# Optimization experiments

Hardware: AMD Instinct MI355X
Metric: run time of the kernel (lower is better)

Reference implementation:

```python
import jax, jax.numpy as jnp
import numpy as np

NEG_FILL = -1.0e9
PROB_MIN = 1e-9


def _lstm_cell(x, h, c, w_ih, w_hh, b_ih, b_hh):
    # PyTorch gate order: input, forget, cell(g), output
    gates = x @ w_ih.T + h @ w_hh.T + b_ih + b_hh
    i, f, g, o = jnp.split(gates, 4, axis=-1)
    c_new = jax.nn.sigmoid(f) * c + jax.nn.sigmoid(i) * jnp.tanh(g)
    h_new = jax.nn.sigmoid(o) * jnp.tanh(c_new)
    return h_new, c_new


def setup_inputs() -> dict:
    key = jax.random.key(0)
    B, T, D, H, W = 2048, 100, 128, 256, 256
    ks = jax.random.split(key, 16)
    s_d = 1.0 / np.sqrt(D)
    s_h = 1.0 / np.sqrt(H)
    s_w = 1.0 / np.sqrt(W)
    return {
        "targets": jax.random.normal(ks[0], (B, T, D), jnp.float32),
        "h0": jax.random.normal(ks[1], (1, B, H), jnp.float32),
        "c0": jax.random.normal(ks[2], (1, B, H), jnp.float32),
        "enc_w_ih": jax.random.normal(ks[3], (4 * H, D), jnp.float32) * s_d,
        "enc_w_hh": jax.random.normal(ks[4], (4 * H, H), jnp.float32) * s_h,
        "enc_b_ih": jax.random.normal(ks[5], (4 * H,), jnp.float32) * s_h,
        "enc_b_hh": jax.random.normal(ks[6], (4 * H,), jnp.float32) * s_h,
        "dec_w_ih": jax.random.normal(ks[7], (4 * H, D), jnp.float32) * s_d,
        "dec_w_hh": jax.random.normal(ks[8], (4 * H, H), jnp.float32) * s_h,
        "dec_b_ih": jax.random.normal(ks[9], (4 * H,), jnp.float32) * s_h,
        "dec_b_hh": jax.random.normal(ks[10], (4 * H,), jnp.float32) * s_h,
        "W1": jax.random.normal(ks[11], (W, H), jnp.float32) * s_h,
        "W2": jax.random.normal(ks[12], (W, H), jnp.float32) * s_h,
        "vt": jax.random.normal(ks[13], (W,), jnp.float32) * s_w,
    }


def reference(targets, h0, c0, enc_w_ih, enc_w_hh, enc_b_ih, enc_b_hh,
              dec_w_ih, dec_w_hh, dec_b_ih, dec_b_hh, W1, W2, vt):
    B, T, D = targets.shape
    H = enc_w_hh.shape[1]

    # ---- encoder LSTM (batch_first, zero initial state) ----
    def enc_step(carry, x_t):
        h, c = carry
        h, c = _lstm_cell(x_t, h, c, enc_w_ih, enc_w_hh, enc_b_ih, enc_b_hh)
        return (h, c), h

    z = jnp.zeros((B, H), targets.dtype)
    _, enc_h = jax.lax.scan(enc_step, (z, z), jnp.swapaxes(targets, 0, 1))
    encoder_states = jnp.swapaxes(enc_h, 0, 1)  # [B, T, H]

    blend1 = encoder_states @ W1.T  # [B, T, W]

    a1 = jnp.arange(B)
    init = (h0[0], c0[0], jnp.zeros((B, T), dtype=bool), jnp.zeros_like(targets[:, 0]))

    def dec_step(carry, _):
        h, c, selected, dec_in = carry
        h, c = _lstm_cell(dec_in, h, c, dec_w_ih, dec_w_hh, dec_b_ih, dec_b_hh)
        blend2 = h @ W2.T                                   # [B, W]
        scores = jnp.tanh(blend1 + blend2[:, None, :]) @ vt  # [B, T]
        scores = jnp.where(selected, NEG_FILL, scores)
        sel = jnp.argmax(scores, axis=-1)                    # [B]
        selected = selected.at[a1, sel].set(True)
        probs = jnp.maximum(jax.nn.softmax(scores, axis=-1), PROB_MIN)
        dec_in = targets[a1, sel]                            # [B, D]
        return (h, c, selected, dec_in), probs

    _, probs = jax.lax.scan(dec_step, init, None, length=T)
    return jnp.swapaxes(probs, 0, 1)  # [B, T, T]
```

## Files before the change

### kernel.cpp

```cpp
#include <hip/hip_runtime.h>
#include <math.h>
#include <stdint.h>

#define BB   2048
#define TT   100
#define DD   128
#define HH   256
#define NEGF -1.0e9f

typedef __attribute__((ext_vector_type(8))) short short8_t;
typedef __attribute__((ext_vector_type(4))) float f32x4;

#define MFMA16(a,b,c) __builtin_amdgcn_mfma_f32_16x16x32_bf16((a),(b),(c),0,0,0)

__device__ __forceinline__ float sigmoidf_(float x){ return 1.0f/(1.0f+expf(-x)); }

__device__ __forceinline__ float tanh_fast(float x){
  x = fminf(15.f, fmaxf(-15.f, x));
  const float e = __expf(x + x);
  return (e - 1.f) * __builtin_amdgcn_rcpf(e + 1.f);
}

__device__ __forceinline__ void bf16_split3(float x, unsigned short &h,
                                            unsigned short &m, unsigned short &l){
  const unsigned u = __float_as_uint(x);
  const unsigned r = u + 0x7FFFu + ((u >> 16) & 1u);
  h = (unsigned short)(r >> 16);
  const float rem = x - __uint_as_float(r & 0xFFFF0000u);
  const unsigned u2 = __float_as_uint(rem);
  const unsigned r2 = u2 + 0x7FFFu + ((u2 >> 16) & 1u);
  m = (unsigned short)(r2 >> 16);
  const float rem2 = rem - __uint_as_float(r2 & 0xFFFF0000u);
  l = (unsigned short)(__float_as_uint(rem2) >> 16);
}

__global__ __launch_bounds__(256) void k_split3(const float* __restrict__ src,
    unsigned short* __restrict__ hi, unsigned short* __restrict__ mi,
    unsigned short* __restrict__ lo, int n){
  const int i = blockIdx.x*256 + threadIdx.x;
  if(i < n){ unsigned short h,m,l; bf16_split3(src[i], h, m, l);
             hi[i]=h; mi[i]=m; lo[i]=l; }
}

__global__ __launch_bounds__(256) void k_zero_i32(int* __restrict__ p, int n){
  int i = blockIdx.x*256 + threadIdx.x;
  if(i < n) p[i] = 0;
}

#define MFMA_X6(aH,aM,aL,bH,bM,bL,acc)            \
  do{ acc = MFMA16(aM, bM, acc);                  \
      acc = MFMA16(aH, bL, acc);                  \
      acc = MFMA16(aL, bH, acc);                  \
      acc = MFMA16(aH, bM, acc);                  \
      acc = MFMA16(aM, bH, acc);                  \
      acc = MFMA16(aH, bH, acc); }while(0)

__global__ __launch_bounds__(128) void k_gates_cell(
    const float* __restrict__ Xp, int ldx,
    const float* __restrict__ Hp,
    const unsigned short* __restrict__ WihH, const unsigned short* __restrict__ WihM,
    const unsigned short* __restrict__ WihL,
    const unsigned short* __restrict__ WhhH, const unsigned short* __restrict__ WhhM,
    const unsigned short* __restrict__ WhhL,
    const float* __restrict__ bih, const float* __restrict__ bhh,
    const float* __restrict__ Cp,
    float* __restrict__ Hout, float* __restrict__ Cout,
    float* __restrict__ Hcopy, int hstride)
{
  __shared__ alignas(16) unsigned short AsH[64*40], AsM[64*40], AsL[64*40];
  __shared__ alignas(16) unsigned short WsH[64*40], WsM[64*40], WsL[64*40];
  const int tid  = threadIdx.x;
  const int lane = tid & 63;
  const int wv   = tid >> 6;
  const int l15  = lane & 15;
  const int l4   = lane >> 4;
  const int j0   = blockIdx.x * 16;
  const int m0   = blockIdx.y * 64;

  f32x4 acc[2][4];
  #pragma unroll
  for(int a=0;a<2;a++)
    #pragma unroll
    for(int s=0;s<4;s++)
      #pragma unroll
      for(int e=0;e<4;e++) acc[a][s][e] = 0.f;

  for(int phase=0; phase<2; phase++){
    const float* Am; int lda;
    const unsigned short *WH, *WM, *WL; int ldw, nt;
    if(phase==0){ if(!Xp) continue; Am=Xp; lda=ldx;
                  WH=WihH; WM=WihM; WL=WihL; ldw=DD; nt=4; }
    else        { if(!Hp) continue; Am=Hp; lda=HH;
                  WH=WhhH; WM=WhhM; WL=WhhL; ldw=HH; nt=8; }
    for(int kt=0; kt<nt; kt++){
      const int k0 = kt*32;
      __syncthreads();
      #pragma unroll
      for(int it=0; it<4; it++){
        const int q  = it*128 + tid;
        const int r  = q >> 3;
        const int kq = (q & 7) << 2;
        const float4 v = *(const float4*)(Am + (size_t)(m0+r)*lda + k0 + kq);
        unsigned short h0,m0_,l0,h1,m1_,l1,h2,m2_,l2,h3,m3_,l3;
        bf16_split3(v.x,h0,m0_,l0); bf16_split3(v.y,h1,m1_,l1);
        bf16_split3(v.z,h2,m2_,l2); bf16_split3(v.w,h3,m3_,l3);
        *(ushort4*)&AsH[r*40+kq] = make_ushort4(h0,h1,h2,h3);
        *(ushort4*)&AsM[r*40+kq] = make_ushort4(m0_,m1_,m2_,m3_);
        *(ushort4*)&AsL[r*40+kq] = make_ushort4(l0,l1,l2,l3);
      }
      #pragma unroll
      for(int half=0; half<3; half++){
        const unsigned short* __restrict__ Wg = (half==0)?WH:((half==1)?WM:WL);
        unsigned short* Ws = (half==0)?WsH:((half==1)?WsM:WsL);
        #pragma unroll
        for(int it=0; it<2; it++){
          const int q  = it*128 + tid;
          const int c  = q >> 2;
          const int kq = (q & 3) << 3;
          const int n  = ((c>>4)*HH) + j0 + (c & 15);
          *(uint4*)&Ws[c*40+kq] = *(const uint4*)(Wg + (size_t)n*ldw + k0 + kq);
        }
      }
      __syncthreads();
      short8_t aH[2], aM[2], aL[2];
      #pragma unroll
      for(int fm=0; fm<2; fm++){
        const int r = wv*32 + fm*16 + l15;
        aH[fm] = *(const short8_t*)&AsH[r*40 + l4*8];
        aM[fm] = *(const short8_t*)&AsM[r*40 + l4*8];
        aL[fm] = *(const short8_t*)&AsL[r*40 + l4*8];
      }
      #pragma unroll
      for(int s=0; s<4; s++){
        const int c = s*16 + l15;
        const short8_t bH = *(const short8_t*)&WsH[c*40 + l4*8];
        const short8_t bM = *(const short8_t*)&WsM[c*40 + l4*8];
        const short8_t bL = *(const short8_t*)&WsL[c*40 + l4*8];
        #pragma unroll
        for(int fm=0; fm<2; fm++){
          MFMA_X6(aH[fm],aM[fm],aL[fm], bH,bM,bL, acc[fm][s]);
        }
      }
    }
  }

  const int j = j0 + l15;
  const float bi0 = bih[       j] + bhh[       j];
  const float bf0 = bih[  HH + j] + bhh[  HH + j];
  const float bg0 = bih[2*HH + j] + bhh[2*HH + j];
  const float bo0 = bih[3*HH + j] + bhh[3*HH + j];
  #pragma unroll
  for(int fm=0; fm<2; fm++){
    #pragma unroll
    for(int r=0; r<4; r++){
      const int m = m0 + wv*32 + fm*16 + l4*4 + r;
      const size_t idx = (size_t)m*HH + j;
      const float iv = acc[fm][0][r] + bi0;
      const float fv = acc[fm][1][r] + bf0;
      const float gv = acc[fm][2][r] + bg0;
      const float ov = acc[fm][3][r] + bo0;
      const float cp = Cp ? Cp[idx] : 0.f;
      const float cn = sigmoidf_(fv)*cp + sigmoidf_(iv)*tanhf(gv);
      const float hn = sigmoidf_(ov)*tanhf(cn);
      Cout[idx] = cn;
      Hout[idx] = hn;
      if(Hcopy) Hcopy[(size_t)m*hstride + j] = hn;
    }
  }
}

__global__ __launch_bounds__(128) void k_blend2(
    const float* __restrict__ Hin,
    const unsigned short* __restrict__ W2H, const unsigned short* __restrict__ W2M,
    const unsigned short* __restrict__ W2L,
    float* __restrict__ out)
{
  __shared__ alignas(16) unsigned short AsH[32*40], AsM[32*40], AsL[32*40];
  __shared__ alignas(16) unsigned short WsH[64*40], WsM[64*40], WsL[64*40];
  const int tid  = threadIdx.x;
  const int lane = tid & 63;
  const int wv   = tid >> 6;
  const int l15  = lane & 15;
  const int l4   = lane >> 4;
  const int n0   = blockIdx.x * 64;
  const int m0   = blockIdx.y * 32;

  f32x4 acc[4];
  #pragma unroll
  for(int s=0;s<4;s++)
    #pragma unroll
    for(int e=0;e<4;e++) acc[s][e] = 0.f;

  for(int kt=0; kt<8; kt++){
    const int k0 = kt*32;
    __syncthreads();
    #pragma unroll
    for(int it=0; it<2; it++){
      const int q  = it*128 + tid;
      const int r  = q >> 3;
      const int kq = (q & 7) << 2;
      const float4 v = *(const float4*)(Hin + (size_t)(m0+r)*HH + k0 + kq);
      unsigned short h0,m0_,l0,h1,m1_,l1,h2,m2_,l2,h3,m3_,l3;
      bf16_split3(v.x,h0,m0_,l0); bf16_split3(v.y,h1,m1_,l1);
      bf16_split3(v.z,h2,m2_,l2); bf16_split3(v.w,h3,m3_,l3);
      *(ushort4*)&AsH[r*40+kq] = make_ushort4(h0,h1,h2,h3);
      *(ushort4*)&AsM[r*40+kq] = make_ushort4(m0_,m1_,m2_,m3_);
      *(ushort4*)&AsL[r*40+kq] = make_ushort4(l0,l1,l2,l3);
    }
    #pragma unroll
    for(int half=0; half<3; half++){
      const unsigned short* __restrict__ Wg = (half==0)?W2H:((half==1)?W2M:W2L);
      unsigned short* Ws = (half==0)?WsH:((half==1)?WsM:WsL);
      #pragma unroll
      for(int it=0; it<2; it++){
        const int q  = it*128 + tid;
        const int c  = q >> 2;
        const int kq = (q & 3) << 3;
        const int n  = n0 + c;
        *(uint4*)&Ws[c*40+kq] = *(const uint4*)(Wg + (size_t)n*HH + k0 + kq);
      }
    }
    __syncthreads();
    const int r = wv*16 + l15;
    const short8_t aH = *(const short8_t*)&AsH[r*40 + l4*8];
    const short8_t aM = *(const short8_t*)&AsM[r*40 + l4*8];
    const short8_t aL = *(const short8_t*)&AsL[r*40 + l4*8];
    #pragma unroll
    for(int s=0; s<4; s++){
      const int c = s*16 + l15;
      const short8_t bH = *(const short8_t*)&WsH[c*40 + l4*8];
      const short8_t bM = *(const short8_t*)&WsM[c*40 + l4*8];
      const short8_t bL = *(const short8_t*)&WsL[c*40 + l4*8];
      MFMA_X6(aH,aM,aL, bH,bM,bL, acc[s]);
    }
  }
  #pragma unroll
  for(int s=0; s<4; s++)
    #pragma unroll
    for(int r=0; r<4; r++)
      out[(size_t)(m0 + wv*16 + l4*4 + r)*HH + n0 + s*16 + l15] = acc[s][r];
}

__global__ __launch_bounds__(128) void k_blend1(
    float* __restrict__ blend1,
    const unsigned short* __restrict__ W1H, const unsigned short* __restrict__ W1M,
    const unsigned short* __restrict__ W1L)
{
  __shared__ alignas(16) unsigned short AsH[32*264], AsM[32*264], AsL[32*264];
  const int tid  = threadIdx.x;
  const int lane = tid & 63;
  const int wv   = tid >> 6;
  const int l15  = lane & 15;
  const int l4   = lane >> 4;
  const size_t r0 = (size_t)blockIdx.x * 32;

  #pragma unroll
  for(int it=0; it<16; it++){
    const int q  = it*128 + tid;
    const int r  = q >> 6;
    const int kq = (q & 63) << 2;
    const float4 v = *(const float4*)(blend1 + (r0+r)*256 + kq);
    unsigned short h0,m0_,l0,h1,m1_,l1,h2,m2_,l2,h3,m3_,l3;
    bf16_split3(v.x,h0,m0_,l0); bf16_split3(v.y,h1,m1_,l1);
    bf16_split3(v.z,h2,m2_,l2); bf16_split3(v.w,h3,m3_,l3);
    *(ushort4*)&AsH[r*264+kq] = make_ushort4(h0,h1,h2,h3);
    *(ushort4*)&AsM[r*264+kq] = make_ushort4(m0_,m1_,m2_,m3_);
    *(ushort4*)&AsL[r*264+kq] = make_ushort4(l0,l1,l2,l3);
  }
  __syncthreads();

  f32x4 acc[16];
  #pragma unroll
  for(int s=0;s<16;s++)
    #pragma unroll
    for(int e=0;e<4;e++) acc[s][e] = 0.f;

  const int rb = wv*16;
  for(int kt=0; kt<8; kt++){
    const int k0 = kt*32;
    const short8_t aH = *(const short8_t*)&AsH[(rb+l15)*264 + k0 + l4*8];
    const short8_t aM = *(const short8_t*)&AsM[(rb+l15)*264 + k0 + l4*8];
    const short8_t aL = *(const short8_t*)&AsL[(rb+l15)*264 + k0 + l4*8];
    #pragma unroll
    for(int fn=0; fn<16; fn++){
      const int n = fn*16 + l15;
      const short8_t bH = *(const short8_t*)(W1H + (size_t)n*256 + k0 + l4*8);
      const short8_t bM = *(const short8_t*)(W1M + (size_t)n*256 + k0 + l4*8);
      const short8_t bL = *(const short8_t*)(W1L + (size_t)n*256 + k0 + l4*8);
      MFMA_X6(aH,aM,aL, bH,bM,bL, acc[fn]);
    }
  }
  #pragma unroll
  for(int fn=0; fn<16; fn++)
    #pragma unroll
    for(int r=0; r<4; r++)
      blend1[(r0 + rb + l4*4 + r)*256 + fn*16 + l15] = acc[fn][r];
}

__global__ __launch_bounds__(256) void k_scores(
    const float* __restrict__ blend1,
    const float* __restrict__ blend2,
    const float* __restrict__ vt,
    const float* __restrict__ targets,
    int*  __restrict__ selected,
    float* __restrict__ dec_in,
    float* __restrict__ out,
    int s)
{
  __shared__ float vt_s[256], b2_s[256], sc[128];
  __shared__ float M_s, S_s;
  __shared__ int sel_s;
  const int b = blockIdx.x;
  const int tid = threadIdx.x;
  const int lane = tid & 63;
  const int wave = tid >> 6;

  vt_s[tid] = vt[tid];
  b2_s[tid] = blend2[(size_t)b*256 + tid];
  __syncthreads();

  const float4 bb = *(const float4*)&b2_s[lane*4];
  const float4 vv = *(const float4*)&vt_s[lane*4];

  for(int it=0; it<25; it++){
    const int t = wave + it*4;
    const float4 x = *(const float4*)(blend1 + ((size_t)b*TT + t)*256 + lane*4);
    float p;
    p = tanh_fast(x.x + bb.x) * vv.x;
    p = fmaf(tanh_fast(x.y + bb.y), vv.y, p);
    p = fmaf(tanh_fast(x.z + bb.z), vv.z, p);
    p = fmaf(tanh_fast(x.w + bb.w), vv.w, p);
    #pragma unroll
    for(int off=32; off>=1; off>>=1) p += __shfl_xor(p, off, 64);
    if(lane == 0) sc[t] = p;
  }
  __syncthreads();

  if(wave == 0){
    float m1 = selected[(size_t)b*TT + lane] ? NEGF : sc[lane];
    sc[lane] = m1;
    float bestv = m1; int besti = lane;
    float m2 = 0.f;
    const int t2 = lane + 64;
    if(t2 < TT){
      m2 = selected[(size_t)b*TT + t2] ? NEGF : sc[t2];
      sc[t2] = m2;
      if(m2 > bestv){ bestv = m2; besti = t2; }
    }
    #pragma unroll
    for(int off=32; off>=1; off>>=1){
      const float ov = __shfl_xor(bestv, off, 64);
      const int   oi = __shfl_xor(besti, off, 64);
      if(ov > bestv || (ov == bestv && oi < besti)){ bestv = ov; besti = oi; }
    }
    float e = __expf(m1 - bestv);
    if(t2 < TT) e += __expf(m2 - bestv);
    #pragma unroll
    for(int off=32; off>=1; off>>=1) e += __shfl_xor(e, off, 64);
    if(lane == 0){
      M_s = bestv; S_s = e; sel_s = besti;
      selected[(size_t)b*TT + besti] = 1;
    }
  }
  __syncthreads();

  const int sel = sel_s;
  if(tid < TT){
    float p = __expf(sc[tid] - M_s) / S_s;
    out[(size_t)b*TT*TT + (size_t)s*TT + tid] = fmaxf(p, 1e-9f);
  }
  if(tid < DD){
    dec_in[(size_t)b*DD + tid] = targets[((size_t)b*TT + sel)*DD + tid];
  }
}

extern "C" void kernel_launch(void* const* d_in, const int* in_sizes, int n_in,
                              void* d_out, int out_size, void* d_ws, size_t ws_size,
                              hipStream_t stream)
{
  (void)in_sizes; (void)n_in; (void)out_size; (void)ws_size;
  const float* targets  = (const float*)d_in[0];
  const float* h0       = (const float*)d_in[1];
  const float* c0       = (const float*)d_in[2];
  const float* enc_w_ih = (const float*)d_in[3];
  const float* enc_w_hh = (const float*)d_in[4];
  const float* enc_b_ih = (const float*)d_in[5];
  const float* enc_b_hh = (const float*)d_in[6];
  const float* dec_w_ih = (const float*)d_in[7];
  const float* dec_w_hh = (const float*)d_in[8];
  const float* dec_b_ih = (const float*)d_in[9];
  const float* dec_b_hh = (const float*)d_in[10];
  const float* W1       = (const float*)d_in[11];
  const float* W2       = (const float*)d_in[12];
  const float* vt       = (const float*)d_in[13];
  float* out = (float*)d_out;

  float* ws      = (float*)d_ws;
  float* blend1  = ws;
  float* hA      = blend1 + (size_t)BB*TT*256;
  float* hB      = hA + (size_t)BB*HH;
  float* cA      = hB + (size_t)BB*HH;
  float* cB      = cA + (size_t)BB*HH;
  float* blend2  = cB + (size_t)BB*HH;
  float* dec_in  = blend2 + (size_t)BB*HH;
  int*   selected= (int*)(dec_in + (size_t)BB*DD);

  char* pc = (char*)(selected + (size_t)BB*TT);
  pc = (char*)(((uintptr_t)pc + 63) & ~(uintptr_t)63);
  unsigned short* q = (unsigned short*)pc;
  unsigned short* ewihH = q; q += (size_t)1024*128;
  unsigned short* ewihM = q; q += (size_t)1024*128;
  unsigned short* ewihL = q; q += (size_t)1024*128;
  unsigned short* ewhhH = q; q += (size_t)1024*256;
  unsigned short* ewhhM = q; q += (size_t)1024*256;
  unsigned short* ewhhL = q; q += (size_t)1024*256;
  unsigned short* dwihH = q; q += (size_t)1024*128;
  unsigned short* dwihM = q; q += (size_t)1024*128;
  unsigned short* dwihL = q; q += (size_t)1024*128;
  unsigned short* dwhhH = q; q += (size_t)1024*256;
  unsigned short* dwhhM = q; q += (size_t)1024*256;
  unsigned short* dwhhL = q; q += (size_t)1024*256;
  unsigned short* w1H   = q; q += (size_t)256*256;
  unsigned short* w1M   = q; q += (size_t)256*256;
  unsigned short* w1L   = q; q += (size_t)256*256;
  unsigned short* w2H   = q; q += (size_t)256*256;
  unsigned short* w2M   = q; q += (size_t)256*256;
  unsigned short* w2L   = q; q += (size_t)256*256;

  k_split3<<<(1024*128+255)/256, 256, 0, stream>>>(enc_w_ih, ewihH, ewihM, ewihL, 1024*128);
  k_split3<<<(1024*256+255)/256, 256, 0, stream>>>(enc_w_hh, ewhhH, ewhhM, ewhhL, 1024*256);
  k_split3<<<(1024*128+255)/256, 256, 0, stream>>>(dec_w_ih, dwihH, dwihM, dwihL, 1024*128);
  k_split3<<<(1024*256+255)/256, 256, 0, stream>>>(dec_w_hh, dwhhH, dwhhM, dwhhL, 1024*256);
  k_split3<<<(256*256+255)/256,  256, 0, stream>>>(W1, w1H, w1M, w1L, 256*256);
  k_split3<<<(256*256+255)/256,  256, 0, stream>>>(W2, w2H, w2M, w2L, 256*256);

  k_zero_i32<<<(BB*TT + 255)/256, 256, 0, stream>>>(selected, BB*TT);

  for(int t=0; t<TT; t++){
    const float* Hp = (t==0) ? nullptr : ((t&1) ? hA : hB);
    const float* Cp = (t==0) ? nullptr : ((t&1) ? cA : cB);
    float* Ho = (t&1) ? hB : hA;
    float* Co = (t&1) ? cB : cA;
    k_gates_cell<<<dim3(16,32), 128, 0, stream>>>(
        targets + (size_t)t*DD, TT*DD,
        Hp, ewihH, ewihM, ewihL, ewhhH, ewhhM, ewhhL, enc_b_ih, enc_b_hh, Cp,
        Ho, Co, blend1 + (size_t)t*256, TT*256);
  }

  k_blend1<<<BB*TT/32, 128, 0, stream>>>(blend1, w1H, w1M, w1L);

  for(int s=0; s<TT; s++){
    const float* Hp = (s==0) ? h0 : ((s&1) ? hA : hB);
    const float* Cp = (s==0) ? c0 : ((s&1) ? cA : cB);
    float* Ho = (s&1) ? hB : hA;
    float* Co = (s&1) ? cB : cA;
    const float* Xp = (s==0) ? nullptr : dec_in;
    k_gates_cell<<<dim3(16,32), 128, 0, stream>>>(
        Xp, DD, Hp, dwihH, dwihM, dwihL, dwhhH, dwhhM, dwhhL, dec_b_ih, dec_b_hh, Cp,
        Ho, Co, nullptr, 0);
    k_blend2<<<dim3(4,64), 128, 0, stream>>>(Ho, w2H, w2M, w2L, blend2);
    k_scores<<<BB, 256, 0, stream>>>(blend1, blend2, vt, targets, selected,
                                     dec_in, out, s);
  }
}
```

Before: 14.68 ms.

## Fuse encoder and decoder time loops into persistent cooperative kernels

```diff
diff --git a/kernel.cpp b/kernel.cpp
--- a/kernel.cpp
+++ b/kernel.cpp
@@ -1,6 +1,9 @@
 #include <hip/hip_runtime.h>
+#include <hip/hip_cooperative_groups.h>
 #include <math.h>
 #include <stdint.h>
+
+namespace cg = cooperative_groups;
 
 #define BB   2048
 #define TT   100
@@ -20,6 +23,8 @@
   const float e = __expf(x + x);
   return (e - 1.f) * __builtin_amdgcn_rcpf(e + 1.f);
 }
+
+__device__ __forceinline__ float b2f(unsigned u){ return __uint_as_float(u << 16); }
 
 __device__ __forceinline__ void bf16_split3(float x, unsigned short &h,
                                             unsigned short &m, unsigned short &l){
@@ -47,6 +52,13 @@
   if(i < n) p[i] = 0;
 }
 
+__global__ __launch_bounds__(256) void k_transpose256(const float* __restrict__ in,
+                                                      float* __restrict__ outp){
+  const int k = blockIdx.x;
+  const int n = threadIdx.x;
+  outp[k*256 + n] = in[n*256 + k];
+}
+
 #define MFMA_X6(aH,aM,aL,bH,bM,bL,acc)            \
   do{ acc = MFMA16(aM, bM, acc);                  \
       acc = MFMA16(aH, bL, acc);                  \
@@ -55,190 +67,376 @@
       acc = MFMA16(aM, bH, acc);                  \
       acc = MFMA16(aH, bH, acc); }while(0)
 
-__global__ __launch_bounds__(128) void k_gates_cell(
-    const float* __restrict__ Xp, int ldx,
-    const float* __restrict__ Hp,
+struct GatesSmem {
+  alignas(16) unsigned short AsH[64*40];
+  alignas(16) unsigned short AsM[64*40];
+  alignas(16) unsigned short AsL[64*40];
+  alignas(16) unsigned short WsH[128*40];
+  alignas(16) unsigned short WsM[128*40];
+  alignas(16) unsigned short WsL[128*40];
+};
+
+__device__ __forceinline__ void stage_W(GatesSmem& sm,
+    const unsigned short* __restrict__ WH, const unsigned short* __restrict__ WM,
+    const unsigned short* __restrict__ WL, int ldw, int j0, int k0, int tid){
+  #pragma unroll
+  for(int half=0; half<3; half++){
+    const unsigned short* __restrict__ Wg = (half==0)?WH:((half==1)?WM:WL);
+    unsigned short* Ws = (half==0)?sm.WsH:((half==1)?sm.WsM:sm.WsL);
+    #pragma unroll
+    for(int it=0; it<2; it++){
+      const int q  = it*256 + tid;
+      const int cc = q >> 2;
+      const int kq = (q & 3) << 3;
+      const int n  = ((cc>>5)*HH) + j0 + (cc & 31);
+      *(uint4*)&Ws[cc*40 + kq] = *(const uint4*)(Wg + (size_t)n*ldw + k0 + kq);
+    }
+  }
+}
+
+__device__ __forceinline__ void stage_A_presplit(GatesSmem& sm,
+    const unsigned short* __restrict__ AH, const unsigned short* __restrict__ AM,
+    const unsigned short* __restrict__ AL, int lda, int m0, int k0, int tid){
+  const int r  = tid >> 2;
+  const int kq = (tid & 3) << 3;
+  const size_t off = (size_t)(m0+r)*lda + k0 + kq;
+  *(uint4*)&sm.AsH[r*40+kq] = *(const uint4*)(AH + off);
+  *(uint4*)&sm.AsM[r*40+kq] = *(const uint4*)(AM + off);
+  *(uint4*)&sm.AsL[r*40+kq] = *(const uint4*)(AL + off);
+}
+
+__device__ __forceinline__ void stage_A_f32(GatesSmem& sm,
+    const float* __restrict__ A, size_t lda, int m0, int k0, int tid){
+  #pragma unroll
+  for(int it=0; it<2; it++){
+    const int q  = it*256 + tid;
+    const int r  = q >> 3;
+    const int kq = (q & 7) << 2;
+    const float4 v = *(const float4*)(A + (size_t)(m0+r)*lda + k0 + kq);
+    unsigned short h0,m0_,l0,h1,m1_,l1,h2,m2_,l2,h3,m3_,l3;
+    bf16_split3(v.x,h0,m0_,l0); bf16_split3(v.y,h1,m1_,l1);
+    bf16_split3(v.z,h2,m2_,l2); bf16_split3(v.w,h3,m3_,l3);
+    *(ushort4*)&sm.AsH[r*40+kq] = make_ushort4(h0,h1,h2,h3);
+    *(ushort4*)&sm.AsM[r*40+kq] = make_ushort4(m0_,m1_,m2_,m3_);
+    *(ushort4*)&sm.AsL[r*40+kq] = make_ushort4(l0,l1,l2,l3);
+  }
+}
+
+__device__ __forceinline__ void gates_compute(GatesSmem& sm, f32x4 (&acc)[2][4],
+                                              int mh, int j16, int l15, int l4){
+  short8_t aH[2], aM[2], aL[2];
+  #pragma unroll
+  for(int fm=0; fm<2; fm++){
+    const int rr = mh*32 + fm*16 + l15;
+    aH[fm] = *(const short8_t*)&sm.AsH[rr*40 + l4*8];
+    aM[fm] = *(const short8_t*)&sm.AsM[rr*40 + l4*8];
+    aL[fm] = *(const short8_t*)&sm.AsL[rr*40 + l4*8];
+  }
+  #pragma unroll
+  for(int s4=0; s4<4; s4++){
+    const int cc = s4*32 + j16 + l15;
+    const short8_t bH = *(const short8_t*)&sm.WsH[cc*40 + l4*8];
+    const short8_t bM = *(const short8_t*)&sm.WsM[cc*40 + l4*8];
+    const short8_t bL = *(const short8_t*)&sm.WsL[cc*40 + l4*8];
+    #pragma unroll
+    for(int fm=0; fm<2; fm++){
+      MFMA_X6(aH[fm],aM[fm],aL[fm], bH,bM,bL, acc[fm][s4]);
+    }
+  }
+}
+
+__global__ __launch_bounds__(256) void k_encoder(
+    const float* __restrict__ targets,
     const unsigned short* __restrict__ WihH, const unsigned short* __restrict__ WihM,
     const unsigned short* __restrict__ WihL,
     const unsigned short* __restrict__ WhhH, const unsigned short* __restrict__ WhhM,
     const unsigned short* __restrict__ WhhL,
     const float* __restrict__ bih, const float* __restrict__ bhh,
-    const float* __restrict__ Cp,
-    float* __restrict__ Hout, float* __restrict__ Cout,
-    float* __restrict__ Hcopy, int hstride)
+    unsigned short* __restrict__ hAH, unsigned short* __restrict__ hAM,
+    unsigned short* __restrict__ hAL,
+    unsigned short* __restrict__ hBH, unsigned short* __restrict__ hBM,
+    unsigned short* __restrict__ hBL,
+    float* __restrict__ cbuf, float* __restrict__ blend1)
 {
-  __shared__ alignas(16) unsigned short AsH[64*40], AsM[64*40], AsL[64*40];
-  __shared__ alignas(16) unsigned short WsH[64*40], WsM[64*40], WsL[64*40];
+  cg::grid_group grid = cg::this_grid();
+  __shared__ GatesSmem sm;
   const int tid  = threadIdx.x;
   const int lane = tid & 63;
   const int wv   = tid >> 6;
   const int l15  = lane & 15;
   const int l4   = lane >> 4;
-  const int j0   = blockIdx.x * 16;
-  const int m0   = blockIdx.y * 64;
-
-  f32x4 acc[2][4];
-  #pragma unroll
-  for(int a=0;a<2;a++)
-    #pragma unroll
-    for(int s=0;s<4;s++)
-      #pragma unroll
-      for(int e=0;e<4;e++) acc[a][s][e] = 0.f;
-
-  for(int phase=0; phase<2; phase++){
-    const float* Am; int lda;
-    const unsigned short *WH, *WM, *WL; int ldw, nt;
-    if(phase==0){ if(!Xp) continue; Am=Xp; lda=ldx;
-                  WH=WihH; WM=WihM; WL=WihL; ldw=DD; nt=4; }
-    else        { if(!Hp) continue; Am=Hp; lda=HH;
-                  WH=WhhH; WM=WhhM; WL=WhhL; ldw=HH; nt=8; }
-    for(int kt=0; kt<nt; kt++){
-      const int k0 = kt*32;
-      __syncthreads();
-      #pragma unroll
-      for(int it=0; it<4; it++){
-        const int q  = it*128 + tid;
-        const int r  = q >> 3;
-        const int kq = (q & 7) << 2;
-        const float4 v = *(const float4*)(Am + (size_t)(m0+r)*lda + k0 + kq);
-        unsigned short h0,m0_,l0,h1,m1_,l1,h2,m2_,l2,h3,m3_,l3;
-        bf16_split3(v.x,h0,m0_,l0); bf16_split3(v.y,h1,m1_,l1);
-        bf16_split3(v.z,h2,m2_,l2); bf16_split3(v.w,h3,m3_,l3);
-        *(ushort4*)&AsH[r*40+kq] = make_ushort4(h0,h1,h2,h3);
-        *(ushort4*)&AsM[r*40+kq] = make_ushort4(m0_,m1_,m2_,m3_);
-        *(ushort4*)&AsL[r*40+kq] = make_ushort4(l0,l1,l2,l3);
-      }
-      #pragma unroll
-      for(int half=0; half<3; half++){
-        const unsigned short* __restrict__ Wg = (half==0)?WH:((half==1)?WM:WL);
-        unsigned short* Ws = (half==0)?WsH:((half==1)?WsM:WsL);
-        #pragma unroll
-        for(int it=0; it<2; it++){
-          const int q  = it*128 + tid;
-          const int c  = q >> 2;
-          const int kq = (q & 3) << 3;
-          const int n  = ((c>>4)*HH) + j0 + (c & 15);
-          *(uint4*)&Ws[c*40+kq] = *(const uint4*)(Wg + (size_t)n*ldw + k0 + kq);
-        }
-      }
-      __syncthreads();
-      short8_t aH[2], aM[2], aL[2];
-      #pragma unroll
-      for(int fm=0; fm<2; fm++){
-        const int r = wv*32 + fm*16 + l15;
-        aH[fm] = *(const short8_t*)&AsH[r*40 + l4*8];
-        aM[fm] = *(const short8_t*)&AsM[r*40 + l4*8];
-        aL[fm] = *(const short8_t*)&AsL[r*40 + l4*8];
-      }
-      #pragma unroll
-      for(int s=0; s<4; s++){
-        const int c = s*16 + l15;
-        const short8_t bH = *(const short8_t*)&WsH[c*40 + l4*8];
-        const short8_t bM = *(const short8_t*)&WsM[c*40 + l4*8];
-        const short8_t bL = *(const short8_t*)&WsL[c*40 + l4*8];
-        #pragma unroll
-        for(int fm=0; fm<2; fm++){
-          MFMA_X6(aH[fm],aM[fm],aL[fm], bH,bM,bL, acc[fm][s]);
-        }
-      }
-    }
-  }
-
-  const int j = j0 + l15;
+  const int bid  = blockIdx.x;
+  const int m0   = (bid >> 3) * 64;
+  const int j0   = (bid & 7) * 32;
+  const int mh   = wv & 1;
+  const int j16  = (wv >> 1) * 16;
+
+  const int j = j0 + j16 + l15;
   const float bi0 = bih[       j] + bhh[       j];
   const float bf0 = bih[  HH + j] + bhh[  HH + j];
   const float bg0 = bih[2*HH + j] + bhh[2*HH + j];
   const float bo0 = bih[3*HH + j] + bhh[3*HH + j];
-  #pragma unroll
-  for(int fm=0; fm<2; fm++){
-    #pragma unroll
-    for(int r=0; r<4; r++){
-      const int m = m0 + wv*32 + fm*16 + l4*4 + r;
-      const size_t idx = (size_t)m*HH + j;
-      const float iv = acc[fm][0][r] + bi0;
-      const float fv = acc[fm][1][r] + bf0;
-      const float gv = acc[fm][2][r] + bg0;
-      const float ov = acc[fm][3][r] + bo0;
-      const float cp = Cp ? Cp[idx] : 0.f;
-      const float cn = sigmoidf_(fv)*cp + sigmoidf_(iv)*tanhf(gv);
-      const float hn = sigmoidf_(ov)*tanhf(cn);
-      Cout[idx] = cn;
-      Hout[idx] = hn;
-      if(Hcopy) Hcopy[(size_t)m*hstride + j] = hn;
-    }
-  }
-}
-
-__global__ __launch_bounds__(128) void k_blend2(
-    const float* __restrict__ Hin,
-    const unsigned short* __restrict__ W2H, const unsigned short* __restrict__ W2M,
-    const unsigned short* __restrict__ W2L,
-    float* __restrict__ out)
+
+  for(int t=0; t<TT; t++){
+    f32x4 acc[2][4];
+    #pragma unroll
+    for(int a=0;a<2;a++)
+      #pragma unroll
+      for(int s=0;s<4;s++)
+        #pragma unroll
+        for(int e=0;e<4;e++) acc[a][s][e] = 0.f;
+
+    for(int kt=0; kt<4; kt++){
+      const int k0 = kt*32;
+      __syncthreads();
+      stage_A_f32(sm, targets + (size_t)t*DD, (size_t)TT*DD, m0, k0, tid);
+      stage_W(sm, WihH, WihM, WihL, DD, j0, k0, tid);
+      __syncthreads();
+      gates_compute(sm, acc, mh, j16, l15, l4);
+    }
+    if(t > 0){
+      const unsigned short* hH = (t&1) ? hAH : hBH;
+      const unsigned short* hM = (t&1) ? hAM : hBM;
+      const unsigned short* hL = (t&1) ? hAL : hBL;
+      for(int kt=0; kt<8; kt++){
+        const int k0 = kt*32;
+        __syncthreads();
+        stage_A_presplit(sm, hH, hM, hL, HH, m0, k0, tid);
+        stage_W(sm, WhhH, WhhM, WhhL, HH, j0, k0, tid);
+        __syncthreads();
+        gates_compute(sm, acc, mh, j16, l15, l4);
+      }
+    }
+    unsigned short* hoH = (t&1) ? hBH : hAH;
+    unsigned short* hoM = (t&1) ? hBM : hAM;
+    unsigned short* hoL = (t&1) ? hBL : hAL;
+    #pragma unroll
+    for(int fm=0; fm<2; fm++){
+      #pragma unroll
+      for(int r=0; r<4; r++){
+        const int m = m0 + mh*32 + fm*16 + l4*4 + r;
+        const size_t idx = (size_t)m*HH + j;
+        const float iv = acc[fm][0][r] + bi0;
+        const float fv = acc[fm][1][r] + bf0;
+        const float gv = acc[fm][2][r] + bg0;
+        const float ov = acc[fm][3][r] + bo0;
+        const float cp = (t==0) ? 0.f : cbuf[idx];
+        const float cn = sigmoidf_(fv)*cp + sigmoidf_(iv)*tanhf(gv);
+        const float hn = sigmoidf_(ov)*tanhf(cn);
+        cbuf[idx] = cn;
+        unsigned short sh, sm_, sl;
+        bf16_split3(hn, sh, sm_, sl);
+        hoH[idx] = sh; hoM[idx] = sm_; hoL[idx] = sl;
+        blend1[(size_t)m*(TT*256) + (size_t)t*256 + j] = hn;
+      }
+    }
+    if(t < TT-1) grid.sync();
+  }
+}
+
+__global__ __launch_bounds__(256) void k_decoder(
+    const float* __restrict__ targets,
+    const unsigned short* __restrict__ WihH, const unsigned short* __restrict__ WihM,
+    const unsigned short* __restrict__ WihL,
+    const unsigned short* __restrict__ WhhH, const unsigned short* __restrict__ WhhM,
+    const unsigned short* __restrict__ WhhL,
+    const float* __restrict__ bih, const float* __restrict__ bhh,
+    const float* __restrict__ c0, float* __restrict__ cbuf,
+    const unsigned short* __restrict__ hAH, const unsigned short* __restrict__ hAM,
+    const unsigned short* __restrict__ hAL,
+    unsigned short* __restrict__ hBH, unsigned short* __restrict__ hBM,
+    unsigned short* __restrict__ hBL,
+    unsigned short* __restrict__ decH, unsigned short* __restrict__ decM,
+    unsigned short* __restrict__ decL,
+    const float* __restrict__ W2t, const float* __restrict__ vt,
+    const float* __restrict__ blend1,
+    int* __restrict__ selected, float* __restrict__ outp)
 {
-  __shared__ alignas(16) unsigned short AsH[32*40], AsM[32*40], AsL[32*40];
-  __shared__ alignas(16) unsigned short WsH[64*40], WsM[64*40], WsL[64*40];
+  cg::grid_group grid = cg::this_grid();
+  __shared__ GatesSmem sm;
+  __shared__ float Hs[8][260];
+  __shared__ float scs[8][104];
   const int tid  = threadIdx.x;
   const int lane = tid & 63;
   const int wv   = tid >> 6;
   const int l15  = lane & 15;
   const int l4   = lane >> 4;
-  const int n0   = blockIdx.x * 64;
-  const int m0   = blockIdx.y * 32;
-
-  f32x4 acc[4];
-  #pragma unroll
-  for(int s=0;s<4;s++)
-    #pragma unroll
-    for(int e=0;e<4;e++) acc[s][e] = 0.f;
-
-  for(int kt=0; kt<8; kt++){
-    const int k0 = kt*32;
+  const int bid  = blockIdx.x;
+  const int m0   = (bid >> 3) * 64;
+  const int j0   = (bid & 7) * 32;
+  const int mh   = wv & 1;
+  const int j16  = (wv >> 1) * 16;
+  const int r0b  = bid * 8;
+
+  const int j = j0 + j16 + l15;
+  const float bi0 = bih[       j] + bhh[       j];
+  const float bf0 = bih[  HH + j] + bhh[  HH + j];
+  const float bg0 = bih[2*HH + j] + bhh[2*HH + j];
+  const float bo0 = bih[3*HH + j] + bhh[3*HH + j];
+  const float4 vv = *(const float4*)(vt + lane*4);
+
+  for(int st=0; st<TT; st++){
+    f32x4 acc[2][4];
+    #pragma unroll
+    for(int a=0;a<2;a++)
+      #pragma unroll
+      for(int s=0;s<4;s++)
+        #pragma unroll
+        for(int e=0;e<4;e++) acc[a][s][e] = 0.f;
+
+    if(st > 0){
+      for(int kt=0; kt<4; kt++){
+        const int k0 = kt*32;
+        __syncthreads();
+        stage_A_presplit(sm, decH, decM, decL, DD, m0, k0, tid);
+        stage_W(sm, WihH, WihM, WihL, DD, j0, k0, tid);
+        __syncthreads();
+        gates_compute(sm, acc, mh, j16, l15, l4);
+      }
+    }
+    {
+      const unsigned short* hH = (st&1) ? hBH : hAH;
+      const unsigned short* hM = (st&1) ? hBM : hAM;
+      const unsigned short* hL = (st&1) ? hBL : hAL;
+      for(int kt=0; kt<8; kt++){
+        const int k0 = kt*32;
+        __syncthreads();
+        stage_A_presplit(sm, hH, hM, hL, HH, m0, k0, tid);
+        stage_W(sm, WhhH, WhhM, WhhL, HH, j0, k0, tid);
+        __syncthreads();
+        gates_compute(sm, acc, mh, j16, l15, l4);
+      }
+    }
+    {
+      unsigned short* hoH = (st&1) ? (unsigned short*)hAH : hBH;
+      unsigned short* hoM = (st&1) ? (unsigned short*)hAM : hBM;
+      unsigned short* hoL = (st&1) ? (unsigned short*)hAL : hBL;
+      const float* csrc = (st==0) ? c0 : cbuf;
+      #pragma unroll
+      for(int fm=0; fm<2; fm++){
+        #pragma unroll
+        for(int r=0; r<4; r++){
+          const int m = m0 + mh*32 + fm*16 + l4*4 + r;
+          const size_t idx = (size_t)m*HH + j;
+          const float iv = acc[fm][0][r] + bi0;
+          const float fv = acc[fm][1][r] + bf0;
+          const float gv = acc[fm][2][r] + bg0;
+          const float ov = acc[fm][3][r] + bo0;
+          const float cp = csrc[idx];
+          const float cn = sigmoidf_(fv)*cp + sigmoidf_(iv)*tanhf(gv);
+          const float hn = sigmoidf_(ov)*tanhf(cn);
+          cbuf[idx] = cn;
+          unsigned short sh, sm_, sl;
+          bf16_split3(hn, sh, sm_, sl);
+          hoH[idx] = sh; hoM[idx] = sm_; hoL[idx] = sl;
+        }
+      }
+    }
+    grid.sync();
+
+    {
+      const unsigned short* hH = (st&1) ? hAH : hBH;
+      const unsigned short* hM = (st&1) ? hAM : hBM;
+      const unsigned short* hL = (st&1) ? hAL : hBL;
+      const int r  = tid >> 5;
+      const int kq = (tid & 31) << 3;
+      const size_t off = (size_t)(r0b + r)*HH + kq;
+      const uint4 uh = *(const uint4*)(hH + off);
+      const uint4 um = *(const uint4*)(hM + off);
+      const uint4 ul = *(const uint4*)(hL + off);
+      #pragma unroll
+      for(int e=0; e<4; e++){
+        const unsigned wh = ((const unsigned*)&uh)[e];
+        const unsigned wm = ((const unsigned*)&um)[e];
+        const unsigned wl = ((const unsigned*)&ul)[e];
+        Hs[r][kq + e*2 + 0] = b2f(wh & 0xffffu) + b2f(wm & 0xffffu) + b2f(wl & 0xffffu);
+        Hs[r][kq + e*2 + 1] = b2f(wh >> 16)     + b2f(wm >> 16)     + b2f(wl >> 16);
+      }
+    }
     __syncthreads();
-    #pragma unroll
-    for(int it=0; it<2; it++){
-      const int q  = it*128 + tid;
-      const int r  = q >> 3;
-      const int kq = (q & 7) << 2;
-      const float4 v = *(const float4*)(Hin + (size_t)(m0+r)*HH + k0 + kq);
-      unsigned short h0,m0_,l0,h1,m1_,l1,h2,m2_,l2,h3,m3_,l3;
-      bf16_split3(v.x,h0,m0_,l0); bf16_split3(v.y,h1,m1_,l1);
-      bf16_split3(v.z,h2,m2_,l2); bf16_split3(v.w,h3,m3_,l3);
-      *(ushort4*)&AsH[r*40+kq] = make_ushort4(h0,h1,h2,h3);
-      *(ushort4*)&AsM[r*40+kq] = make_ushort4(m0_,m1_,m2_,m3_);
-      *(ushort4*)&AsL[r*40+kq] = make_ushort4(l0,l1,l2,l3);
-    }
-    #pragma unroll
-    for(int half=0; half<3; half++){
-      const unsigned short* __restrict__ Wg = (half==0)?W2H:((half==1)?W2M:W2L);
-      unsigned short* Ws = (half==0)?WsH:((half==1)?WsM:WsL);
-      #pragma unroll
-      for(int it=0; it<2; it++){
-        const int q  = it*128 + tid;
-        const int c  = q >> 2;
-        const int kq = (q & 3) << 3;
-        const int n  = n0 + c;
-        *(uint4*)&Ws[c*40+kq] = *(const uint4*)(Wg + (size_t)n*HH + k0 + kq);
-      }
-    }
-    __syncthreads();
-    const int r = wv*16 + l15;
-    const short8_t aH = *(const short8_t*)&AsH[r*40 + l4*8];
-    const short8_t aM = *(const short8_t*)&AsM[r*40 + l4*8];
-    const short8_t aL = *(const short8_t*)&AsL[r*40 + l4*8];
-    #pragma unroll
-    for(int s=0; s<4; s++){
-      const int c = s*16 + l15;
-      const short8_t bH = *(const short8_t*)&WsH[c*40 + l4*8];
-      const short8_t bM = *(const short8_t*)&WsM[c*40 + l4*8];
-      const short8_t bL = *(const short8_t*)&WsL[c*40 + l4*8];
-      MFMA_X6(aH,aM,aL, bH,bM,bL, acc[s]);
-    }
-  }
-  #pragma unroll
-  for(int s=0; s<4; s++)
-    #pragma unroll
-    for(int r=0; r<4; r++)
-      out[(size_t)(m0 + wv*16 + l4*4 + r)*HH + n0 + s*16 + l15] = acc[s][r];
+
+    float bacc[2][4];
+    #pragma unroll
+    for(int r=0;r<2;r++)
+      #pragma unroll
+      for(int cG=0;cG<4;cG++) bacc[r][cG] = 0.f;
+    {
+      const int rA = wv*2, rB = wv*2 + 1;
+      for(int kc=0; kc<64; kc++){
+        const float4 ha = *(const float4*)&Hs[rA][kc*4];
+        const float4 hb = *(const float4*)&Hs[rB][kc*4];
+        const float haa[4] = {ha.x,ha.y,ha.z,ha.w};
+        const float hbb[4] = {hb.x,hb.y,hb.z,hb.w};
+        #pragma unroll
+        for(int i=0;i<4;i++){
+          const float4 w = *(const float4*)(W2t + (size_t)(kc*4+i)*HH + lane*4);
+          bacc[0][0] = fmaf(haa[i], w.x, bacc[0][0]);
+          bacc[0][1] = fmaf(haa[i], w.y, bacc[0][1]);
+          bacc[0][2] = fmaf(haa[i], w.z, bacc[0][2]);
+          bacc[0][3] = fmaf(haa[i], w.w, bacc[0][3]);
+          bacc[1][0] = fmaf(hbb[i], w.x, bacc[1][0]);
+          bacc[1][1] = fmaf(hbb[i], w.y, bacc[1][1]);
+          bacc[1][2] = fmaf(hbb[i], w.z, bacc[1][2]);
+          bacc[1][3] = fmaf(hbb[i], w.w, bacc[1][3]);
+        }
+      }
+    }
+
+    #pragma unroll
+    for(int rr=0; rr<2; rr++){
+      const int r = wv*2 + rr;
+      const int brow = r0b + r;
+      const float4 bb = make_float4(bacc[rr][0], bacc[rr][1], bacc[rr][2], bacc[rr][3]);
+      const float* bl = blend1 + (size_t)brow * (TT*256);
+      #pragma unroll 2
+      for(int t=0; t<TT; t++){
+        const float4 x = *(const float4*)(bl + t*256 + lane*4);
+        float p;
+        p = tanh_fast(x.x + bb.x) * vv.x;
+        p = fmaf(tanh_fast(x.y + bb.y), vv.y, p);
+        p = fmaf(tanh_fast(x.z + bb.z), vv.z, p);
+        p = fmaf(tanh_fast(x.w + bb.w), vv.w, p);
+        #pragma unroll
+        for(int off=32; off>=1; off>>=1) p += __shfl_xor(p, off, 64);
+        if(lane == 0) scs[r][t] = p;
+      }
+      const size_t selbase = (size_t)brow*TT;
+      const float m1 = selected[selbase + lane] ? NEGF : scs[r][lane];
+      float bestv = m1; int besti = lane;
+      const int t2 = lane + 64;
+      float m2 = NEGF;
+      if(t2 < TT){
+        m2 = selected[selbase + t2] ? NEGF : scs[r][t2];
+        if(m2 > bestv){ bestv = m2; besti = t2; }
+      }
+      #pragma unroll
+      for(int off=32; off>=1; off>>=1){
+        const float ov = __shfl_xor(bestv, off, 64);
+        const int   oi = __shfl_xor(besti, off, 64);
+        if(ov > bestv || (ov == bestv && oi < besti)){ bestv = ov; besti = oi; }
+      }
+      float e = __expf(m1 - bestv);
+      if(t2 < TT) e += __expf(m2 - bestv);
+      #pragma unroll
+      for(int off=32; off>=1; off>>=1) e += __shfl_xor(e, off, 64);
+
+      outp[(size_t)brow*(TT*TT) + (size_t)st*TT + lane] = fmaxf(__expf(m1 - bestv)/e, 1e-9f);
+      if(t2 < TT)
+        outp[(size_t)brow*(TT*TT) + (size_t)st*TT + t2] = fmaxf(__expf(m2 - bestv)/e, 1e-9f);
+      if(lane == 0) selected[selbase + besti] = 1;
+      #pragma unroll
+      for(int dd=0; dd<2; dd++){
+        const int d = lane + dd*64;
+        const float xv = targets[((size_t)brow*TT + besti)*DD + d];
+        unsigned short th, tm, tl;
+        bf16_split3(xv, th, tm, tl);
+        decH[(size_t)brow*DD + d] = th;
+        decM[(size_t)brow*DD + d] = tm;
+        decL[(size_t)brow*DD + d] = tl;
+      }
+    }
+    if(st < TT-1) grid.sync();
+  }
 }
 
 __global__ __launch_bounds__(128) void k_blend1(
@@ -295,83 +493,6 @@
     #pragma unroll
     for(int r=0; r<4; r++)
       blend1[(r0 + rb + l4*4 + r)*256 + fn*16 + l15] = acc[fn][r];
-}
-
-__global__ __launch_bounds__(256) void k_scores(
-    const float* __restrict__ blend1,
-    const float* __restrict__ blend2,
-    const float* __restrict__ vt,
-    const float* __restrict__ targets,
-    int*  __restrict__ selected,
-    float* __restrict__ dec_in,
-    float* __restrict__ out,
-    int s)
-{
-  __shared__ float vt_s[256], b2_s[256], sc[128];
-  __shared__ float M_s, S_s;
-  __shared__ int sel_s;
-  const int b = blockIdx.x;
-  const int tid = threadIdx.x;
-  const int lane = tid & 63;
-  const int wave = tid >> 6;
-
-  vt_s[tid] = vt[tid];
-  b2_s[tid] = blend2[(size_t)b*256 + tid];
-  __syncthreads();
-
-  const float4 bb = *(const float4*)&b2_s[lane*4];
-  const float4 vv = *(const float4*)&vt_s[lane*4];
-
-  for(int it=0; it<25; it++){
-    const int t = wave + it*4;
-    const float4 x = *(const float4*)(blend1 + ((size_t)b*TT + t)*256 + lane*4);
-    float p;
-    p = tanh_fast(x.x + bb.x) * vv.x;
-    p = fmaf(tanh_fast(x.y + bb.y), vv.y, p);
-    p = fmaf(tanh_fast(x.z + bb.z), vv.z, p);
-    p = fmaf(tanh_fast(x.w + bb.w), vv.w, p);
-    #pragma unroll
-    for(int off=32; off>=1; off>>=1) p += __shfl_xor(p, off, 64);
-    if(lane == 0) sc[t] = p;
-  }
-  __syncthreads();
-
-  if(wave == 0){
-    float m1 = selected[(size_t)b*TT + lane] ? NEGF : sc[lane];
-    sc[lane] = m1;
-    float bestv = m1; int besti = lane;
-    float m2 = 0.f;
-    const int t2 = lane + 64;
-    if(t2 < TT){
-      m2 = selected[(size_t)b*TT + t2] ? NEGF : sc[t2];
-      sc[t2] = m2;
-      if(m2 > bestv){ bestv = m2; besti = t2; }
-    }
-    #pragma unroll
-    for(int off=32; off>=1; off>>=1){
-      const float ov = __shfl_xor(bestv, off, 64);
-      const int   oi = __shfl_xor(besti, off, 64);
-      if(ov > bestv || (ov == bestv && oi < besti)){ bestv = ov; besti = oi; }
-    }
-    float e = __expf(m1 - bestv);
-    if(t2 < TT) e += __expf(m2 - bestv);
-    #pragma unroll
-    for(int off=32; off>=1; off>>=1) e += __shfl_xor(e, off, 64);
-    if(lane == 0){
-      M_s = bestv; S_s = e; sel_s = besti;
-      selected[(size_t)b*TT + besti] = 1;
-    }
-  }
-  __syncthreads();
-
-  const int sel = sel_s;
-  if(tid < TT){
-    float p = __expf(sc[tid] - M_s) / S_s;
-    out[(size_t)b*TT*TT + (size_t)s*TT + tid] = fmaxf(p, 1e-9f);
-  }
-  if(tid < DD){
-    dec_in[(size_t)b*DD + tid] = targets[((size_t)b*TT + sel)*DD + tid];
-  }
 }
 
 extern "C" void kernel_launch(void* const* d_in, const int* in_sizes, int n_in,
@@ -393,21 +514,22 @@
   const float* W1       = (const float*)d_in[11];
   const float* W2       = (const float*)d_in[12];
   const float* vt       = (const float*)d_in[13];
-  float* out = (float*)d_out;
+  float* outp = (float*)d_out;
 
   float* ws      = (float*)d_ws;
   float* blend1  = ws;
-  float* hA      = blend1 + (size_t)BB*TT*256;
-  float* hB      = hA + (size_t)BB*HH;
-  float* cA      = hB + (size_t)BB*HH;
-  float* cB      = cA + (size_t)BB*HH;
-  float* blend2  = cB + (size_t)BB*HH;
-  float* dec_in  = blend2 + (size_t)BB*HH;
-  int*   selected= (int*)(dec_in + (size_t)BB*DD);
-
+  float* cbuf    = blend1 + (size_t)BB*TT*256;
+  float* W2t     = cbuf + (size_t)BB*HH;
+  int*   selected= (int*)(W2t + 256*256);
   char* pc = (char*)(selected + (size_t)BB*TT);
   pc = (char*)(((uintptr_t)pc + 63) & ~(uintptr_t)63);
   unsigned short* q = (unsigned short*)pc;
+  unsigned short* hsAH = q; q += (size_t)BB*HH;
+  unsigned short* hsAM = q; q += (size_t)BB*HH;
+  unsigned short* hsAL = q; q += (size_t)BB*HH;
+  unsigned short* hsBH = q; q += (size_t)BB*HH;
+  unsigned short* hsBM = q; q += (size_t)BB*HH;
+  unsigned short* hsBL = q; q += (size_t)BB*HH;
   unsigned short* ewihH = q; q += (size_t)1024*128;
   unsigned short* ewihM = q; q += (size_t)1024*128;
   unsigned short* ewihL = q; q += (size_t)1024*128;
@@ -423,43 +545,49 @@
   unsigned short* w1H   = q; q += (size_t)256*256;
   unsigned short* w1M   = q; q += (size_t)256*256;
   unsigned short* w1L   = q; q += (size_t)256*256;
-  unsigned short* w2H   = q; q += (size_t)256*256;
-  unsigned short* w2M   = q; q += (size_t)256*256;
-  unsigned short* w2L   = q; q += (size_t)256*256;
+  unsigned short* decH = ewihH;
+  unsigned short* decM = ewihH + (size_t)BB*DD;
+  unsigned short* decL = ewihH + (size_t)2*BB*DD;
 
   k_split3<<<(1024*128+255)/256, 256, 0, stream>>>(enc_w_ih, ewihH, ewihM, ewihL, 1024*128);
   k_split3<<<(1024*256+255)/256, 256, 0, stream>>>(enc_w_hh, ewhhH, ewhhM, ewhhL, 1024*256);
   k_split3<<<(1024*128+255)/256, 256, 0, stream>>>(dec_w_ih, dwihH, dwihM, dwihL, 1024*128);
   k_split3<<<(1024*256+255)/256, 256, 0, stream>>>(dec_w_hh, dwhhH, dwhhM, dwhhL, 1024*256);
   k_split3<<<(256*256+255)/256,  256, 0, stream>>>(W1, w1H, w1M, w1L, 256*256);
-  k_split3<<<(256*256+255)/256,  256, 0, stream>>>(W2, w2H, w2M, w2L, 256*256);
-
+  k_transpose256<<<256, 256, 0, stream>>>(W2, W2t);
   k_zero_i32<<<(BB*TT + 255)/256, 256, 0, stream>>>(selected, BB*TT);
 
-  for(int t=0; t<TT; t++){
-    const float* Hp = (t==0) ? nullptr : ((t&1) ? hA : hB);
-    const float* Cp = (t==0) ? nullptr : ((t&1) ? cA : cB);
-    float* Ho = (t&1) ? hB : hA;
-    float* Co = (t&1) ? cB : cA;
-    k_gates_cell<<<dim3(16,32), 128, 0, stream>>>(
-        targets + (size_t)t*DD, TT*DD,
-        Hp, ewihH, ewihM, ewihL, ewhhH, ewhhM, ewhhL, enc_b_ih, enc_b_hh, Cp,
-        Ho, Co, blend1 + (size_t)t*256, TT*256);
+  {
+    void* args[] = {
+      (void*)&targets,
+      (void*)&ewihH, (void*)&ewihM, (void*)&ewihL,
+      (void*)&ewhhH, (void*)&ewhhM, (void*)&ewhhL,
+      (void*)&enc_b_ih, (void*)&enc_b_hh,
+      (void*)&hsAH, (void*)&hsAM, (void*)&hsAL,
+      (void*)&hsBH, (void*)&hsBM, (void*)&hsBL,
+      (void*)&cbuf, (void*)&blend1
+    };
+    hipLaunchCooperativeKernel((void*)k_encoder, dim3(256), dim3(256), args, 0, stream);
   }
 
   k_blend1<<<BB*TT/32, 128, 0, stream>>>(blend1, w1H, w1M, w1L);
 
-  for(int s=0; s<TT; s++){
-    const float* Hp = (s==0) ? h0 : ((s&1) ? hA : hB);
-    const float* Cp = (s==0) ? c0 : ((s&1) ? cA : cB);
-    float* Ho = (s&1) ? hB : hA;
-    float* Co = (s&1) ? cB : cA;
-    const float* Xp = (s==0) ? nullptr : dec_in;
-    k_gates_cell<<<dim3(16,32), 128, 0, stream>>>(
-        Xp, DD, Hp, dwihH, dwihM, dwihL, dwhhH, dwhhM, dwhhL, dec_b_ih, dec_b_hh, Cp,
-        Ho, Co, nullptr, 0);
-    k_blend2<<<dim3(4,64), 128, 0, stream>>>(Ho, w2H, w2M, w2L, blend2);
-    k_scores<<<BB, 256, 0, stream>>>(blend1, blend2, vt, targets, selected,
-                                     dec_in, out, s);
-  }
-}
+  k_split3<<<(BB*HH+255)/256, 256, 0, stream>>>(h0, hsAH, hsAM, hsAL, BB*HH);
+
+  {
+    void* args[] = {
+      (void*)&targets,
+      (void*)&dwihH, (void*)&dwihM, (void*)&dwihL,
+      (void*)&dwhhH, (void*)&dwhhM, (void*)&dwhhL,
+      (void*)&dec_b_ih, (void*)&dec_b_hh,
+      (void*)&c0, (void*)&cbuf,
+      (void*)&hsAH, (void*)&hsAM, (void*)&hsAL,
+      (void*)&hsBH, (void*)&hsBM, (void*)&hsBL,
+      (void*)&decH, (void*)&decM, (void*)&decL,
+      (void*)&W2t, (void*)&vt,
+      (void*)&blend1,
+      (void*)&selected, (void*)&outp
+    };
+    hipLaunchCooperativeKernel((void*)k_decoder, dim3(256), dim3(256), args, 0, stream);
+  }
+}
```

After: 27.17 ms. +85.1%, slower.
